# Kernel optimization log

Hardware: AMD Instinct MI355X
Metric: run time of the kernel (lower is better)

## Reference

```python
import jax, jax.numpy as jnp
import numpy as np

B, T, K, U, C, M, H = 64, 600, 10, 64, 54, 20, 512
OUT = 1 + 6 * M        # 121
IN1 = 3 + C            # 57  -> rnn_cell1 input
IN2 = 3 + C + H        # 569 -> rnn_cell2 input
BIAS = 0.0
EPS = 1e-20


def setup_inputs() -> dict:
    key = jax.random.key(0)
    ks = jax.random.split(key, 20)
    p = lambda k, shape: (jax.random.normal(k, shape, dtype=jnp.float32) * 0.05)
    return {
        "x": jax.random.normal(ks[0], (B, T, 3), dtype=jnp.float32),
        "y": jax.random.uniform(ks[1], (B, T, 3), dtype=jnp.float32),
        "c_vec": jax.random.uniform(ks[2], (B, U, C), dtype=jnp.float32),
        "W_ih1": p(ks[3], (4 * H, IN1)), "W_hh1": p(ks[4], (4 * H, H)),
        "b_ih1": p(ks[5], (4 * H,)),     "b_hh1": p(ks[6], (4 * H,)),
        "W_ih2": p(ks[7], (4 * H, IN2)), "W_hh2": p(ks[8], (4 * H, H)),
        "b_ih2": p(ks[9], (4 * H,)),     "b_hh2": p(ks[10], (4 * H,)),
        "W_k": p(ks[11], (3 * K, H)),    "b_k": p(ks[12], (3 * K,)),
        "W_o": p(ks[13], (OUT, H)),      "b_o": p(ks[14], (OUT,)),
    }


def _lstm_cell(xin, h, c, Wih, Whh, bih, bhh):
    g = xin @ Wih.T + h @ Whh.T + bih + bhh          # [B, 4H]
    i, f, gg, o = jnp.split(g, 4, axis=1)            # PyTorch LSTMCell gate order
    c = jax.nn.sigmoid(f) * c + jax.nn.sigmoid(i) * jnp.tanh(gg)
    h = jax.nn.sigmoid(o) * jnp.tanh(c)
    return h, c


def _forward(x, y, c_vec, W_ih1, W_hh1, b_ih1, b_hh1, W_ih2, W_hh2, b_ih2, b_hh2,
             W_k, b_k, W_o, b_o):
    u = jnp.arange(U, dtype=jnp.float32)[None, None, :]   # [1,1,U]
    zB = jnp.zeros((B, H), dtype=x.dtype)

    def step(carry, xt):
        h1, c1, h2, c2, w, kappa = carry
        h1, c1 = _lstm_cell(jnp.concatenate([xt, w], 1), h1, c1, W_ih1, W_hh1, b_ih1, b_hh1)
        kg = h1 @ W_k.T + b_k                               # [B, 3K]
        a_hat, be_hat, ka_hat = jnp.split(kg, 3, axis=1)
        alpha = jnp.exp(a_hat)[:, :, None]                  # [B,K,1]
        beta = jnp.exp(be_hat)[:, :, None]
        kappa = kappa + jnp.exp(ka_hat)[:, :, None]
        phi = jnp.sum(jnp.exp(-beta * (kappa - u) ** 2) * alpha, axis=1)  # [B,U]
        w = jnp.einsum('bu,buc->bc', phi, c_vec)            # [B,C]
        h2, c2 = _lstm_cell(jnp.concatenate([xt, h1, w], 1), h2, c2, W_ih2, W_hh2, b_ih2, b_hh2)
        return (h1, c1, h2, c2, w, kappa), h2

    init = (zB, zB, zB, zB, jnp.zeros((B, C), x.dtype), jnp.zeros((B, K, 1), x.dtype))
    _, h2_seq = jax.lax.scan(step, init, jnp.transpose(x, (1, 0, 2)))   # [T,B,H]
    h2_seq = jnp.transpose(h2_seq, (1, 0, 2)).reshape(-1, H)            # [B*T,H]
    outputs = h2_seq @ W_o.T + b_o                                      # [B*T,OUT]

    y1, y2, s = jnp.moveaxis(y.reshape(-1, 3), 1, 0)                    # each [B*T]
    e = jax.nn.sigmoid(-outputs[:, 0])                                  # 1/(1+exp(o0))
    pi_hat, mu1, mu2, s1_hat, s2_hat, rho_hat = jnp.split(outputs[:, 1:], 6, axis=1)
    pi = jax.nn.softmax(pi_hat, axis=1)
    sigma1 = jnp.exp(s1_hat - BIAS)
    sigma2 = jnp.exp(s2_hat - BIAS)
    rho = jnp.tanh(rho_hat)
    d1 = (y1[:, None] - mu1) / sigma1
    d2 = (y2[:, None] - mu2) / sigma2
    z = d1 ** 2 + d2 ** 2 - 2.0 * rho * d1 * d2
    one_m_r2 = 1.0 - rho ** 2
    gauss = jnp.exp(-z / (2.0 * one_m_r2)) / (2.0 * np.pi * sigma1 * sigma2 * jnp.sqrt(one_m_r2))
    loss_g = jnp.sum(-jnp.log(jnp.sum(pi * gauss, axis=1) + EPS))
    loss_b = jnp.sum(-jnp.log((e + EPS) * s + (1.0 - e + EPS) * (1.0 - s)))
    return (loss_g + loss_b) / (B * T)


def reference(x, y, c_vec, W_ih1, W_hh1, b_ih1, b_hh1, W_ih2, W_hh2, b_ih2, b_hh2,
              W_k, b_k, W_o, b_o):
    return _forward(x, y, c_vec, W_ih1, W_hh1, b_ih1, b_hh1, W_ih2, W_hh2,
                    b_ih2, b_hh2, W_k, b_k, W_o, b_o)
```

## Files before the change

### kernel.cpp

```cpp
#include <hip/hip_runtime.h>
#include <math.h>

typedef _Float16 f16;
typedef _Float16 f16x8 __attribute__((ext_vector_type(8)));
typedef float f32x4 __attribute__((ext_vector_type(4)));
union AFU { unsigned long long q[2]; f16x8 v; };
union HU { f16 h; unsigned short u; };

#define NT 512
#define NBLK 160
#define AROW 1088
#define ABE 69632
#define OUTG_OFF 69632
#define LOSS_OFF 77824
#define BAR_OFF  78080
#define PH_STRIDE 144
#define NPH 1206
#define DYN_LDS 132096

__device__ __forceinline__ unsigned long long ald64(const void* p) {
  return __hip_atomic_load((const unsigned long long*)p, __ATOMIC_RELAXED, __HIP_MEMORY_SCOPE_AGENT);
}
__device__ __forceinline__ unsigned ald32(const void* p) {
  return __hip_atomic_load((const unsigned*)p, __ATOMIC_RELAXED, __HIP_MEMORY_SCOPE_AGENT);
}
__device__ __forceinline__ void ast32(void* p, unsigned v) {
  __hip_atomic_store((unsigned*)p, v, __ATOMIC_RELAXED, __HIP_MEMORY_SCOPE_AGENT);
}
__device__ __forceinline__ float sigm(float v){ return 1.f/(1.f+expf(-v)); }

__device__ __forceinline__ void gbar(unsigned* bar, int p) {
  asm volatile("s_waitcnt vmcnt(0)" ::: "memory");
  __syncthreads();
  if (threadIdx.x == 0) {
    unsigned* base = bar + p * PH_STRIDE;
    unsigned a = __hip_atomic_fetch_add(base + (blockIdx.x & 7) * 16, 1u,
                                        __ATOMIC_RELAXED, __HIP_MEMORY_SCOPE_AGENT);
    if (a == 19u)
      __hip_atomic_fetch_add(base + 128, 1u, __ATOMIC_RELAXED, __HIP_MEMORY_SCOPE_AGENT);
    while (__hip_atomic_load(base + 128, __ATOMIC_RELAXED, __HIP_MEMORY_SCOPE_AGENT) < 8u) {}
  }
  __syncthreads();
}

__device__ __forceinline__ float mix_loss(const float* so, const float* yl, int t, int m) {
  float y1 = yl[t*3+0], y2 = yl[t*3+1], ys = yl[t*3+2];
  float ph = (m < 20) ? so[1+m] : -1e30f;
  float mx = ph;
  #pragma unroll
  for (int d = 16; d >= 1; d >>= 1) mx = fmaxf(mx, __shfl_xor(mx, d));
  float pe = (m < 20) ? expf(ph - mx) : 0.f;
  float ps = pe;
  #pragma unroll
  for (int d = 16; d >= 1; d >>= 1) ps += __shfl_xor(ps, d);
  float contrib = 0.f;
  if (m < 20) {
    float mu1 = so[21+m], mu2 = so[41+m];
    float s1 = expf(so[61+m]), s2 = expf(so[81+m]);
    float rh = tanhf(so[101+m]);
    float d1 = (y1-mu1)/s1, d2 = (y2-mu2)/s2;
    float omr = 1.f - rh*rh;
    float z = d1*d1 + d2*d2 - 2.f*rh*d1*d2;
    float ga = expf(-z/(2.f*omr)) / (6.283185307179586f * s1 * s2 * sqrtf(omr));
    contrib = (pe/ps)*ga;
  }
  float gs = contrib;
  #pragma unroll
  for (int d = 16; d >= 1; d >>= 1) gs += __shfl_xor(gs, d);
  float lg = -logf(gs + 1e-20f);
  float e = 1.f/(1.f + expf(so[0]));
  float lb = -logf((e + 1e-20f)*ys + (1.f - e + 1e-20f)*(1.f - ys));
  return lg + lb;
}

__global__ __launch_bounds__(256) void k_init(float* ws) {
  unsigned* w0 = (unsigned*)ws;
  unsigned* wb = (unsigned*)ws + BAR_OFF;
  int idx = blockIdx.x*256 + threadIdx.x;
  int str = gridDim.x*256;
  for (int e = idx; e < ABE; e += str) w0[e] = 0u;
  for (int e = idx; e < NPH*PH_STRIDE; e += str) wb[e] = 0u;
}

__global__ __launch_bounds__(NT, 1) void kmain(
    const float* __restrict__ x, const float* __restrict__ y, const float* __restrict__ cvec,
    const float* __restrict__ Wih1, const float* __restrict__ Whh1,
    const float* __restrict__ bih1, const float* __restrict__ bhh1,
    const float* __restrict__ Wih2, const float* __restrict__ Whh2,
    const float* __restrict__ bih2, const float* __restrict__ bhh2,
    const float* __restrict__ Wk, const float* __restrict__ bk,
    const float* __restrict__ Wo, const float* __restrict__ bo,
    float* __restrict__ out, float* __restrict__ ws)
{
  extern __shared__ char dsm[];
  const int blk = blockIdx.x, tid = threadIdx.x;
  const int wv = tid >> 6, l = tid & 63;

  f16* AB = (f16*)ws;
  float* outg  = ws + OUTG_OFF;
  float* lossg = ws + LOSS_OFF;
  unsigned* bar = (unsigned*)ws + BAR_OFF;

  float lreg = 0.f;

  if (blk < 64) {
    f16* wf2 = (f16*)dsm;
    for (int f = tid; f < 2*34*64; f += NT) {
      int nt = f / (34*64), rem = f - nt*34*64, j = rem >> 6, lf = rem & 63;
      int nrow = nt*16 + (lf & 15);
      int R = (nrow >> 3)*512 + blk*8 + (nrow & 7);
      int kbase = j*32 + (lf >> 4)*8;
      #pragma unroll
      for (int e = 0; e < 8; ++e) {
        int k = kbase + e;
        float v = 0.f;
        if (k >= 4 && k < 58)        v = Wih2[R*569 + 515 + (k-4)];
        else if (k >= 58 && k < 61)  v = Wih2[R*569 + (k-58)];
        else if (k >= 64 && k < 576) v = Wih2[R*569 + 3 + (k-64)];
        else if (k >= 576)           v = Whh2[R*512 + (k-576)];
        wf2[f*8 + e] = (f16)v;
      }
    }
  } else if (blk < 96) {
    const int g1i = blk - 64;
    f16* wf1  = (f16*)dsm;
    f16* wofr = (f16*)(dsm + 73728);
    for (int f = tid; f < 4*18*64; f += NT) {
      int nt = f / (18*64), rem = f - nt*18*64, j = rem >> 6, lf = rem & 63;
      int nrow = nt*16 + (lf & 15);
      int R = (nrow >> 4)*512 + g1i*16 + (nrow & 15);
      int kbase = j*32 + (lf >> 4)*8;
      #pragma unroll
      for (int e = 0; e < 8; ++e) {
        int k = kbase + e;
        float v = 0.f;
        if (k < 3)                   v = Wih1[R*57 + k];
        else if (k >= 4 && k < 58)   v = Wih1[R*57 + 3 + (k-4)];
        else if (k >= 64 && k < 576) v = Whh1[R*512 + (k-64)];
        wf1[f*8 + e] = (f16)v;
      }
    }
    for (int f = tid; f < 16*64; f += NT) {
      int j = f >> 6, lf = f & 63;
      int nrow = lf & 15, row = g1i*4 + nrow;
      int kbase = j*32 + (lf >> 4)*8;
      #pragma unroll
      for (int e = 0; e < 8; ++e) {
        float v = (nrow < 4 && row < 121) ? Wo[row*512 + kbase + e] : 0.f;
        wofr[f*8 + e] = (f16)v;
      }
    }
  } else {
    const int b = blk - 96;
    f16*   wk  = (f16*)dsm;
    float* cv  = (float*)(dsm + 31200);
    float* xl  = (float*)(dsm + 45024);
    float* yl  = (float*)(dsm + 52224);
    for (int e = tid; e < 30*512; e += NT) { int j = e >> 9, k = e & 511; wk[j*520 + k] = (f16)Wk[e]; }
    for (int e = tid; e < 3456; e += NT) cv[e] = cvec[b*3456 + e];
    for (int e = tid; e < 1800; e += NT) { xl[e] = x[b*1800+e]; yl[e] = y[b*1800+e]; }
    float* kap = (float*)(dsm + 61152);
    if (tid < 10) kap[tid] = 0.f;
    __syncthreads();
    if (tid == 0) {
      HU h0, h1u, h2u;
      h0.h = (f16)xl[0]; h1u.h = (f16)xl[1]; h2u.h = (f16)xl[2];
      ast32((unsigned*)AB + (b*1088 >> 1),       (unsigned)h0.u | ((unsigned)h1u.u << 16));
      ast32((unsigned*)AB + ((b*1088 + 2) >> 1), (unsigned)h2u.u);
    }
  }

  float bias_g[4] = {0,0,0,0}, bias1a[4] = {0,0,0,0}, bias1b[4] = {0,0,0,0};
  float borow = 0.f;
  float c_st = 0.f, c1a = 0.f, c1b = 0.f;
  if (blk < 64) {
    int pr = tid & 7;
    #pragma unroll
    for (int g = 0; g < 4; ++g) {
      int R = g*512 + blk*8 + pr;
      bias_g[g] = bih2[R] + bhh2[R];
    }
  } else if (blk < 96) {
    int g1i = blk - 64, pr = tid & 7;
    #pragma unroll
    for (int g = 0; g < 4; ++g) {
      int Ra = g*512 + g1i*16 + 2*pr, Rb = Ra + 1;
      bias1a[g] = bih1[Ra] + bhh1[Ra];
      bias1b[g] = bih1[Rb] + bhh1[Rb];
    }
    int r = tid >> 6;
    if (r < 4) { int row = g1i*4 + r; borow = (row < 121) ? bo[row] : 0.f; }
  }

  gbar(bar, 0);

  for (int i = 0; i <= 601; ++i) {
    const f16* __restrict__ Acur = AB + (i & 1)*ABE;
    f16* __restrict__ Anxt = AB + ((i & 1)^1)*ABE;
    unsigned* AnxtW = (unsigned*)Anxt;

    if (blk < 64) {
      if (i >= 1 && i <= 600) {
        f16* wf2 = (f16*)dsm;
        float* part2 = (float*)(dsm + 69632);
        const int mt = wv & 3, kh = wv >> 2;
        const int mA = mt*16 + (l & 15);
        const int kb = (l >> 4)*8;
        const f16* Ap = Acur + mA*1088;
        f32x4 acc0 = {0,0,0,0}, acc1 = {0,0,0,0};
        #pragma unroll
        for (int jj = 0; jj < 17; ++jj) {
          int j = kh*17 + jj;
          int k = j*32 + kb;
          AFU af;
          af.q[0] = ald64(Ap + k);
          af.q[1] = ald64(Ap + k + 4);
          f16x8 b0 = *(const f16x8*)&wf2[((0*34 + j)*64 + l)*8];
          f16x8 b1 = *(const f16x8*)&wf2[((1*34 + j)*64 + l)*8];
          acc0 = __builtin_amdgcn_mfma_f32_16x16x32_f16(af.v, b0, acc0, 0, 0, 0);
          acc1 = __builtin_amdgcn_mfma_f32_16x16x32_f16(af.v, b1, acc1, 0, 0, 0);
        }
        #pragma unroll
        for (int r = 0; r < 4; ++r) {
          int m = mt*16 + (l>>4)*4 + r;
          part2[(kh*64 + m)*33 + (l & 15)]      = acc0[r];
          part2[(kh*64 + m)*33 + 16 + (l & 15)] = acc1[r];
        }
        __syncthreads();
        {
          int b_ = tid >> 3, pr = tid & 7;
          const float* p0 = &part2[(0*64 + b_)*33];
          const float* p1 = &part2[(1*64 + b_)*33];
          float gi_ = p0[0*8+pr] + p1[0*8+pr] + bias_g[0];
          float gf_ = p0[1*8+pr] + p1[1*8+pr] + bias_g[1];
          float gg_ = p0[2*8+pr] + p1[2*8+pr] + bias_g[2];
          float go_ = p0[3*8+pr] + p1[3*8+pr] + bias_g[3];
          float ig = sigm(gi_), fg = sigm(gf_), gg2 = tanhf(gg_), og = sigm(go_);
          c_st = fg*c_st + ig*gg2;
          HU hu; hu.h = (f16)(og * tanhf(c_st));
          unsigned myv = hu.u;
          unsigned other = (unsigned)__shfl_xor((int)myv, 1);
          if ((pr & 1) == 0)
            ast32(AnxtW + ((b_*1088 + 576 + blk*8 + pr) >> 1), myv | (other << 16));
        }
      }
    } else if (blk < 96) {
      const int g1i = blk - 64;
      f16* wf1  = (f16*)dsm;
      f16* wofr = (f16*)(dsm + 73728);
      float* part1 = (float*)(dsm + 90112);
      float* partp = (float*)(dsm + 123392);
      bool do_g1 = (i <= 599), do_pr = (i >= 2);
      const int mt = wv & 3, kh = wv >> 2;
      const int mA = mt*16 + (l & 15);
      const int kb = (l >> 4)*8;
      if (do_g1) {
        const f16* Ap = Acur + mA*1088;
        f32x4 acc[4];
        #pragma unroll
        for (int nt = 0; nt < 4; ++nt) acc[nt] = (f32x4){0,0,0,0};
        #pragma unroll
        for (int jj = 0; jj < 9; ++jj) {
          int j = kh*9 + jj;
          int k = j*32 + kb;
          AFU af;
          af.q[0] = ald64(Ap + k);
          af.q[1] = ald64(Ap + k + 4);
          #pragma unroll
          for (int nt = 0; nt < 4; ++nt) {
            f16x8 bf = *(const f16x8*)&wf1[((nt*18 + j)*64 + l)*8];
            acc[nt] = __builtin_amdgcn_mfma_f32_16x16x32_f16(af.v, bf, acc[nt], 0, 0, 0);
          }
        }
        #pragma unroll
        for (int nt = 0; nt < 4; ++nt)
          #pragma unroll
          for (int r = 0; r < 4; ++r) {
            int m = mt*16 + (l>>4)*4 + r;
            part1[(kh*64 + m)*65 + nt*16 + (l & 15)] = acc[nt][r];
          }
      }
      if (do_pr) {
        const f16* Ap = Acur + mA*1088 + 576;
        f32x4 accp = {0,0,0,0};
        #pragma unroll
        for (int jj = 0; jj < 8; ++jj) {
          int j = kh*8 + jj;
          int k = j*32 + kb;
          AFU af;
          af.q[0] = ald64(Ap + k);
          af.q[1] = ald64(Ap + k + 4);
          f16x8 bf = *(const f16x8*)&wofr[(j*64 + l)*8];
          accp = __builtin_amdgcn_mfma_f32_16x16x32_f16(af.v, bf, accp, 0, 0, 0);
        }
        #pragma unroll
        for (int r = 0; r < 4; ++r) {
          int m = mt*16 + (l>>4)*4 + r;
          partp[(kh*64 + m)*17 + (l & 15)] = accp[r];
        }
      }
      if (do_g1 || do_pr) __syncthreads();
      if (do_g1) {
        int b_ = tid >> 3, pr = tid & 7;
        const float* p0 = &part1[(0*64 + b_)*65];
        const float* p1 = &part1[(1*64 + b_)*65];
        float giA = p0[0*16+2*pr] + p1[0*16+2*pr] + bias1a[0];
        float gfA = p0[1*16+2*pr] + p1[1*16+2*pr] + bias1a[1];
        float ggA = p0[2*16+2*pr] + p1[2*16+2*pr] + bias1a[2];
        float goA = p0[3*16+2*pr] + p1[3*16+2*pr] + bias1a[3];
        c1a = sigm(gfA)*c1a + sigm(giA)*tanhf(ggA);
        float hA = sigm(goA) * tanhf(c1a);
        float giB = p0[0*16+2*pr+1] + p1[0*16+2*pr+1] + bias1b[0];
        float gfB = p0[1*16+2*pr+1] + p1[1*16+2*pr+1] + bias1b[1];
        float ggB = p0[2*16+2*pr+1] + p1[2*16+2*pr+1] + bias1b[2];
        float goB = p0[3*16+2*pr+1] + p1[3*16+2*pr+1] + bias1b[3];
        c1b = sigm(gfB)*c1b + sigm(giB)*tanhf(ggB);
        float hB = sigm(goB) * tanhf(c1b);
        HU ua, ub; ua.h = (f16)hA; ub.h = (f16)hB;
        ast32(AnxtW + ((b_*1088 + 64 + g1i*16 + 2*pr) >> 1),
              (unsigned)ua.u | ((unsigned)ub.u << 16));
      }
      if (do_pr && tid < 256) {
        int b_ = tid & 63, r = tid >> 6;
        int row = g1i*4 + r;
        if (row < 121) {
          float v = partp[(0*64 + b_)*17 + r] + partp[(1*64 + b_)*17 + r] + borow;
          unsigned uu; __builtin_memcpy(&uu, &v, 4);
          ast32((unsigned*)outg + b_*128 + row, uu);
        }
      }
    }
    gbar(bar, 1 + 2*i);

    if (blk >= 96) {
      const int b = blk - 96;
      f16*   wk   = (f16*)dsm;
      float* cv   = (float*)(dsm + 31200);
      float* xl   = (float*)(dsm + 45024);
      float* yl   = (float*)(dsm + 52224);
      f16*   h1h  = (f16*)(dsm + 59424);
      float* so   = (float*)(dsm + 60448);
      float* skg  = (float*)(dsm + 60944);
      float* sal  = (float*)(dsm + 61072);
      float* sbe  = (float*)(dsm + 61112);
      float* kap  = (float*)(dsm + 61152);
      float* sphi = (float*)(dsm + 61192);
      float* wtmp = (float*)(dsm + 61448);
      if (i <= 599) {
        if (tid < 64)
          ((unsigned long long*)h1h)[tid] = ald64(Anxt + b*1088 + 64 + tid*4);
        __syncthreads();
        {
          int j = tid >> 4, ksv = tid & 15;
          float a = 0.f;
          if (j < 30) {
            const f16* wr = &wk[j*520 + ksv*32];
            const f16* hr = &h1h[ksv*32];
            #pragma unroll
            for (int c = 0; c < 4; ++c) {
              f16x8 q = *(const f16x8*)(wr + c*8);
              f16x8 h = *(const f16x8*)(hr + c*8);
              #pragma unroll
              for (int e = 0; e < 8; ++e) a += (float)q[e] * (float)h[e];
            }
          }
          a += __shfl_xor(a, 1); a += __shfl_xor(a, 2);
          a += __shfl_xor(a, 4); a += __shfl_xor(a, 8);
          if (j < 30 && ksv == 0) skg[j] = a + bk[j];
        }
        __syncthreads();
        if (tid < 10) {
          sal[tid] = expf(skg[tid]);
          sbe[tid] = expf(skg[10+tid]);
          kap[tid] += expf(skg[20+tid]);
        }
        __syncthreads();
        if (tid < 64) {
          float u = (float)tid, ph = 0.f;
          #pragma unroll
          for (int k2 = 0; k2 < 10; ++k2) {
            float d = kap[k2] - u;
            ph += sal[k2]*expf(-sbe[k2]*d*d);
          }
          sphi[tid] = ph;
        }
        __syncthreads();
        if (tid < 54) {
          float wvv = 0.f;
          #pragma unroll 8
          for (int u = 0; u < 64; ++u) wvv += sphi[u]*cv[u*54 + tid];
          wtmp[tid] = wvv;
        }
        __syncthreads();
        if (tid < 27) {
          HU a, bu; a.h = (f16)wtmp[2*tid]; bu.h = (f16)wtmp[2*tid+1];
          ast32(AnxtW + ((b*1088 + 4 + 2*tid) >> 1), (unsigned)a.u | ((unsigned)bu.u << 16));
        } else if (tid == 27) {
          HU a, bu; a.h = (f16)xl[i*3+0]; bu.h = (f16)xl[i*3+1];
          ast32(AnxtW + ((b*1088 + 58) >> 1), (unsigned)a.u | ((unsigned)bu.u << 16));
        } else if (tid == 28) {
          HU a; a.h = (f16)xl[i*3+2];
          ast32(AnxtW + ((b*1088 + 60) >> 1), (unsigned)a.u);
        } else if (tid == 29 && i <= 598) {
          HU a, bu; a.h = (f16)xl[(i+1)*3+0]; bu.h = (f16)xl[(i+1)*3+1];
          ast32(AnxtW + ((b*1088) >> 1), (unsigned)a.u | ((unsigned)bu.u << 16));
        } else if (tid == 30 && i <= 598) {
          HU a; a.h = (f16)xl[(i+1)*3+2];
          ast32(AnxtW + ((b*1088 + 2) >> 1), (unsigned)a.u);
        }
      }
      if (i >= 2) {
        if (tid < 121) {
          unsigned uu = ald32((unsigned*)outg + b*128 + tid);
          float v; __builtin_memcpy(&v, &uu, 4);
          so[tid] = v;
        }
        __syncthreads();
        if (tid < 32) {
          float v = mix_loss(so, yl, i-2, tid);
          if (tid == 0) lreg += v;
        }
      }
    }
    gbar(bar, 2 + 2*i);
  }

  if (blk >= 96 && tid == 0) {
    unsigned uu; __builtin_memcpy(&uu, &lreg, 4);
    ast32((unsigned*)lossg + (blk - 96), uu);
  }
  gbar(bar, 1205);
  if (blk == 96 && tid < 64) {
    unsigned uu = ald32((unsigned*)lossg + tid);
    float v; __builtin_memcpy(&v, &uu, 4);
    #pragma unroll
    for (int d = 32; d >= 1; d >>= 1) v += __shfl_xor(v, d);
    if (tid == 0) out[0] = v / 38400.f;
  }
}

extern "C" void kernel_launch(void* const* d_in, const int* in_sizes, int n_in,
                              void* d_out, int out_size, void* d_ws, size_t ws_size,
                              hipStream_t stream)
{
  (void)in_sizes; (void)n_in; (void)out_size; (void)ws_size;
  const float* x    = (const float*)d_in[0];
  const float* y    = (const float*)d_in[1];
  const float* cvec = (const float*)d_in[2];
  const float* Wih1 = (const float*)d_in[3];
  const float* Whh1 = (const float*)d_in[4];
  const float* bih1 = (const float*)d_in[5];
  const float* bhh1 = (const float*)d_in[6];
  const float* Wih2 = (const float*)d_in[7];
  const float* Whh2 = (const float*)d_in[8];
  const float* bih2 = (const float*)d_in[9];
  const float* bhh2 = (const float*)d_in[10];
  const float* Wk   = (const float*)d_in[11];
  const float* bk   = (const float*)d_in[12];
  const float* Wo   = (const float*)d_in[13];
  const float* bo   = (const float*)d_in[14];
  float* out = (float*)d_out;
  float* wsf = (float*)d_ws;

  hipFuncSetAttribute((const void*)kmain, hipFuncAttributeMaxDynamicSharedMemorySize, DYN_LDS);

  k_init<<<256, 256, 0, stream>>>(wsf);

  void* args[] = {
    (void*)&x, (void*)&y, (void*)&cvec,
    (void*)&Wih1, (void*)&Whh1, (void*)&bih1, (void*)&bhh1,
    (void*)&Wih2, (void*)&Whh2, (void*)&bih2, (void*)&bhh2,
    (void*)&Wk, (void*)&bk, (void*)&Wo, (void*)&bo,
    (void*)&out, (void*)&wsf
  };
  hipLaunchCooperativeKernel((void*)kmain, dim3(NBLK), dim3(NT), args, DYN_LDS, stream);
}
```

Measured before the change: 10.71 ms.

## Replace atomic counter grid barrier with per-block flag array and batched coherent loads

Swaps the hierarchical fetch-add grid barrier for a per-block monotonically increasing flag that every block polls with vectorized cache-bypassing loads. The relaxed 64-bit atomic loads of activations become 128-bit loads with sc0 sc1 bits, all issued before a single wait so the MFMA loops no longer stall on each load. Stores also use inline-asm coherent stores. The aim is to cut barrier latency and global-load latency on the 1200-step recurrent critical path. The cost is more polling traffic per barrier and reliance on inline-asm cache bits for coherence.

```diff
diff --git a/kernel.cpp b/kernel.cpp
--- a/kernel.cpp
+++ b/kernel.cpp
@@ -4,41 +4,54 @@
 typedef _Float16 f16;
 typedef _Float16 f16x8 __attribute__((ext_vector_type(8)));
 typedef float f32x4 __attribute__((ext_vector_type(4)));
-union AFU { unsigned long long q[2]; f16x8 v; };
 union HU { f16 h; unsigned short u; };
 
 #define NT 512
 #define NBLK 160
-#define AROW 1088
 #define ABE 69632
 #define OUTG_OFF 69632
 #define LOSS_OFF 77824
-#define BAR_OFF  78080
-#define PH_STRIDE 144
-#define NPH 1206
+#define FLAG_OFF 78080
 #define DYN_LDS 132096
 
-__device__ __forceinline__ unsigned long long ald64(const void* p) {
-  return __hip_atomic_load((const unsigned long long*)p, __ATOMIC_RELAXED, __HIP_MEMORY_SCOPE_AGENT);
-}
-__device__ __forceinline__ unsigned ald32(const void* p) {
-  return __hip_atomic_load((const unsigned*)p, __ATOMIC_RELAXED, __HIP_MEMORY_SCOPE_AGENT);
-}
-__device__ __forceinline__ void ast32(void* p, unsigned v) {
-  __hip_atomic_store((unsigned*)p, v, __ATOMIC_RELAXED, __HIP_MEMORY_SCOPE_AGENT);
-}
+__device__ __forceinline__ f16x8 cld16(const void* p) {
+  f16x8 r;
+  asm volatile("global_load_dwordx4 %0, %1, off sc0 sc1" : "=v"(r) : "v"(p) : "memory");
+  return r;
+}
+__device__ __forceinline__ uint4 cld128u(const void* p) {
+  uint4 r;
+  asm volatile("global_load_dwordx4 %0, %1, off sc0 sc1"
+               : "=v"(r) : "v"(p) : "memory");
+  return r;
+}
+__device__ __forceinline__ unsigned cld32u(const void* p) {
+  unsigned r;
+  asm volatile("global_load_dword %0, %1, off sc0 sc1" : "=v"(r) : "v"(p) : "memory");
+  return r;
+}
+__device__ __forceinline__ void cst32(void* p, unsigned v) {
+  asm volatile("global_store_dword %0, %1, off sc0 sc1" :: "v"(p), "v"(v) : "memory");
+}
+#define VMWAIT() do { asm volatile("s_waitcnt vmcnt(0)" ::: "memory"); \
+                      __builtin_amdgcn_sched_barrier(0); } while (0)
+
 __device__ __forceinline__ float sigm(float v){ return 1.f/(1.f+expf(-v)); }
 
-__device__ __forceinline__ void gbar(unsigned* bar, int p) {
+__device__ __forceinline__ void gbar(unsigned* flags, unsigned target) {
   asm volatile("s_waitcnt vmcnt(0)" ::: "memory");
   __syncthreads();
-  if (threadIdx.x == 0) {
-    unsigned* base = bar + p * PH_STRIDE;
-    unsigned a = __hip_atomic_fetch_add(base + (blockIdx.x & 7) * 16, 1u,
-                                        __ATOMIC_RELAXED, __HIP_MEMORY_SCOPE_AGENT);
-    if (a == 19u)
-      __hip_atomic_fetch_add(base + 128, 1u, __ATOMIC_RELAXED, __HIP_MEMORY_SCOPE_AGENT);
-    while (__hip_atomic_load(base + 128, __ATOMIC_RELAXED, __HIP_MEMORY_SCOPE_AGENT) < 8u) {}
+  if (threadIdx.x == 0) cst32(flags + blockIdx.x, target);
+  if (threadIdx.x < 64) {
+    bool ok;
+    do {
+      uint4 vv; vv.x = vv.y = vv.z = vv.w = target;
+      if (threadIdx.x < 40) {
+        vv = cld128u(flags + threadIdx.x * 4);
+        asm volatile("s_waitcnt vmcnt(0)" ::: "memory");
+      }
+      ok = (vv.x >= target) && (vv.y >= target) && (vv.z >= target) && (vv.w >= target);
+    } while (!__all(ok));
   }
   __syncthreads();
 }
@@ -75,11 +88,11 @@
 
 __global__ __launch_bounds__(256) void k_init(float* ws) {
   unsigned* w0 = (unsigned*)ws;
-  unsigned* wb = (unsigned*)ws + BAR_OFF;
+  unsigned* wb = (unsigned*)ws + FLAG_OFF;
   int idx = blockIdx.x*256 + threadIdx.x;
   int str = gridDim.x*256;
   for (int e = idx; e < ABE; e += str) w0[e] = 0u;
-  for (int e = idx; e < NPH*PH_STRIDE; e += str) wb[e] = 0u;
+  if (idx < NBLK) wb[idx] = 0u;
 }
 
 __global__ __launch_bounds__(NT, 1) void kmain(
@@ -99,7 +112,7 @@
   f16* AB = (f16*)ws;
   float* outg  = ws + OUTG_OFF;
   float* lossg = ws + LOSS_OFF;
-  unsigned* bar = (unsigned*)ws + BAR_OFF;
+  unsigned* flags = (unsigned*)ws + FLAG_OFF;
 
   float lreg = 0.f;
 
@@ -165,8 +178,8 @@
     if (tid == 0) {
       HU h0, h1u, h2u;
       h0.h = (f16)xl[0]; h1u.h = (f16)xl[1]; h2u.h = (f16)xl[2];
-      ast32((unsigned*)AB + (b*1088 >> 1),       (unsigned)h0.u | ((unsigned)h1u.u << 16));
-      ast32((unsigned*)AB + ((b*1088 + 2) >> 1), (unsigned)h2u.u);
+      cst32((unsigned*)AB + (b*1088 >> 1),       (unsigned)h0.u | ((unsigned)h1u.u << 16));
+      cst32((unsigned*)AB + ((b*1088 + 2) >> 1), (unsigned)h2u.u);
     }
   }
 
@@ -192,7 +205,7 @@
     if (r < 4) { int row = g1i*4 + r; borow = (row < 121) ? bo[row] : 0.f; }
   }
 
-  gbar(bar, 0);
+  gbar(flags, 1);
 
   for (int i = 0; i <= 601; ++i) {
     const f16* __restrict__ Acur = AB + (i & 1)*ABE;
@@ -208,17 +221,20 @@
         const int kb = (l >> 4)*8;
         const f16* Ap = Acur + mA*1088;
         f32x4 acc0 = {0,0,0,0}, acc1 = {0,0,0,0};
+        f16x8 fr[17];
         #pragma unroll
         for (int jj = 0; jj < 17; ++jj) {
           int j = kh*17 + jj;
-          int k = j*32 + kb;
-          AFU af;
-          af.q[0] = ald64(Ap + k);
-          af.q[1] = ald64(Ap + k + 4);
+          fr[jj] = cld16(Ap + j*32 + kb);
+        }
+        VMWAIT();
+        #pragma unroll
+        for (int jj = 0; jj < 17; ++jj) {
+          int j = kh*17 + jj;
           f16x8 b0 = *(const f16x8*)&wf2[((0*34 + j)*64 + l)*8];
           f16x8 b1 = *(const f16x8*)&wf2[((1*34 + j)*64 + l)*8];
-          acc0 = __builtin_amdgcn_mfma_f32_16x16x32_f16(af.v, b0, acc0, 0, 0, 0);
-          acc1 = __builtin_amdgcn_mfma_f32_16x16x32_f16(af.v, b1, acc1, 0, 0, 0);
+          acc0 = __builtin_amdgcn_mfma_f32_16x16x32_f16(fr[jj], b0, acc0, 0, 0, 0);
+          acc1 = __builtin_amdgcn_mfma_f32_16x16x32_f16(fr[jj], b1, acc1, 0, 0, 0);
         }
         #pragma unroll
         for (int r = 0; r < 4; ++r) {
@@ -241,7 +257,7 @@
           unsigned myv = hu.u;
           unsigned other = (unsigned)__shfl_xor((int)myv, 1);
           if ((pr & 1) == 0)
-            ast32(AnxtW + ((b_*1088 + 576 + blk*8 + pr) >> 1), myv | (other << 16));
+            cst32(AnxtW + ((b_*1088 + 576 + blk*8 + pr) >> 1), myv | (other << 16));
         }
       }
     } else if (blk < 96) {
@@ -254,22 +270,35 @@
       const int mt = wv & 3, kh = wv >> 2;
       const int mA = mt*16 + (l & 15);
       const int kb = (l >> 4)*8;
+      f16x8 fr1[9], frp[8];
       if (do_g1) {
         const f16* Ap = Acur + mA*1088;
-        f32x4 acc[4];
-        #pragma unroll
-        for (int nt = 0; nt < 4; ++nt) acc[nt] = (f32x4){0,0,0,0};
         #pragma unroll
         for (int jj = 0; jj < 9; ++jj) {
           int j = kh*9 + jj;
-          int k = j*32 + kb;
-          AFU af;
-          af.q[0] = ald64(Ap + k);
-          af.q[1] = ald64(Ap + k + 4);
+          fr1[jj] = cld16(Ap + j*32 + kb);
+        }
+      }
+      if (do_pr) {
+        const f16* Ap = Acur + mA*1088 + 576;
+        #pragma unroll
+        for (int jj = 0; jj < 8; ++jj) {
+          int j = kh*8 + jj;
+          frp[jj] = cld16(Ap + j*32 + kb);
+        }
+      }
+      VMWAIT();
+      if (do_g1) {
+        f32x4 acc[4];
+        #pragma unroll
+        for (int nt = 0; nt < 4; ++nt) acc[nt] = (f32x4){0,0,0,0};
+        #pragma unroll
+        for (int jj = 0; jj < 9; ++jj) {
+          int j = kh*9 + jj;
           #pragma unroll
           for (int nt = 0; nt < 4; ++nt) {
             f16x8 bf = *(const f16x8*)&wf1[((nt*18 + j)*64 + l)*8];
-            acc[nt] = __builtin_amdgcn_mfma_f32_16x16x32_f16(af.v, bf, acc[nt], 0, 0, 0);
+            acc[nt] = __builtin_amdgcn_mfma_f32_16x16x32_f16(fr1[jj], bf, acc[nt], 0, 0, 0);
           }
         }
         #pragma unroll
@@ -281,17 +310,12 @@
           }
       }
       if (do_pr) {
-        const f16* Ap = Acur + mA*1088 + 576;
         f32x4 accp = {0,0,0,0};
         #pragma unroll
         for (int jj = 0; jj < 8; ++jj) {
           int j = kh*8 + jj;
-          int k = j*32 + kb;
-          AFU af;
-          af.q[0] = ald64(Ap + k);
-          af.q[1] = ald64(Ap + k + 4);
           f16x8 bf = *(const f16x8*)&wofr[(j*64 + l)*8];
-          accp = __builtin_amdgcn_mfma_f32_16x16x32_f16(af.v, bf, accp, 0, 0, 0);
+          accp = __builtin_amdgcn_mfma_f32_16x16x32_f16(frp[jj], bf, accp, 0, 0, 0);
         }
         #pragma unroll
         for (int r = 0; r < 4; ++r) {
@@ -317,7 +341,7 @@
         c1b = sigm(gfB)*c1b + sigm(giB)*tanhf(ggB);
         float hB = sigm(goB) * tanhf(c1b);
         HU ua, ub; ua.h = (f16)hA; ub.h = (f16)hB;
-        ast32(AnxtW + ((b_*1088 + 64 + g1i*16 + 2*pr) >> 1),
+        cst32(AnxtW + ((b_*1088 + 64 + g1i*16 + 2*pr) >> 1),
               (unsigned)ua.u | ((unsigned)ub.u << 16));
       }
       if (do_pr && tid < 256) {
@@ -326,11 +350,11 @@
         if (row < 121) {
           float v = partp[(0*64 + b_)*17 + r] + partp[(1*64 + b_)*17 + r] + borow;
           unsigned uu; __builtin_memcpy(&uu, &v, 4);
-          ast32((unsigned*)outg + b_*128 + row, uu);
-        }
-      }
-    }
-    gbar(bar, 1 + 2*i);
+          cst32((unsigned*)outg + b_*128 + row, uu);
+        }
+      }
+    }
+    gbar(flags, 2 + 2*i);
 
     if (blk >= 96) {
       const int b = blk - 96;
@@ -347,8 +371,11 @@
       float* sphi = (float*)(dsm + 61192);
       float* wtmp = (float*)(dsm + 61448);
       if (i <= 599) {
-        if (tid < 64)
-          ((unsigned long long*)h1h)[tid] = ald64(Anxt + b*1088 + 64 + tid*4);
+        if (tid < 64) {
+          f16x8 hv = cld16(Anxt + b*1088 + 64 + tid*8);
+          asm volatile("s_waitcnt vmcnt(0)" ::: "memory");
+          *(f16x8*)&h1h[tid*8] = hv;
+        }
         __syncthreads();
         {
           int j = tid >> 4, ksv = tid & 15;
@@ -394,24 +421,25 @@
         __syncthreads();
         if (tid < 27) {
           HU a, bu; a.h = (f16)wtmp[2*tid]; bu.h = (f16)wtmp[2*tid+1];
-          ast32(AnxtW + ((b*1088 + 4 + 2*tid) >> 1), (unsigned)a.u | ((unsigned)bu.u << 16));
+          cst32(AnxtW + ((b*1088 + 4 + 2*tid) >> 1), (unsigned)a.u | ((unsigned)bu.u << 16));
         } else if (tid == 27) {
           HU a, bu; a.h = (f16)xl[i*3+0]; bu.h = (f16)xl[i*3+1];
-          ast32(AnxtW + ((b*1088 + 58) >> 1), (unsigned)a.u | ((unsigned)bu.u << 16));
+          cst32(AnxtW + ((b*1088 + 58) >> 1), (unsigned)a.u | ((unsigned)bu.u << 16));
         } else if (tid == 28) {
           HU a; a.h = (f16)xl[i*3+2];
-          ast32(AnxtW + ((b*1088 + 60) >> 1), (unsigned)a.u);
+          cst32(AnxtW + ((b*1088 + 60) >> 1), (unsigned)a.u);
         } else if (tid == 29 && i <= 598) {
           HU a, bu; a.h = (f16)xl[(i+1)*3+0]; bu.h = (f16)xl[(i+1)*3+1];
-          ast32(AnxtW + ((b*1088) >> 1), (unsigned)a.u | ((unsigned)bu.u << 16));
+          cst32(AnxtW + ((b*1088) >> 1), (unsigned)a.u | ((unsigned)bu.u << 16));
         } else if (tid == 30 && i <= 598) {
           HU a; a.h = (f16)xl[(i+1)*3+2];
-          ast32(AnxtW + ((b*1088 + 2) >> 1), (unsigned)a.u);
+          cst32(AnxtW + ((b*1088 + 2) >> 1), (unsigned)a.u);
         }
       }
       if (i >= 2) {
         if (tid < 121) {
-          unsigned uu = ald32((unsigned*)outg + b*128 + tid);
+          unsigned uu = cld32u((unsigned*)outg + b*128 + tid);
+          asm volatile("s_waitcnt vmcnt(0)" ::: "memory");
           float v; __builtin_memcpy(&v, &uu, 4);
           so[tid] = v;
         }
@@ -422,16 +450,17 @@
         }
       }
     }
-    gbar(bar, 2 + 2*i);
+    gbar(flags, 3 + 2*i);
   }
 
   if (blk >= 96 && tid == 0) {
     unsigned uu; __builtin_memcpy(&uu, &lreg, 4);
-    ast32((unsigned*)lossg + (blk - 96), uu);
-  }
-  gbar(bar, 1205);
+    cst32((unsigned*)lossg + (blk - 96), uu);
+  }
+  gbar(flags, 1206);
   if (blk == 96 && tid < 64) {
-    unsigned uu = ald32((unsigned*)lossg + tid);
+    unsigned uu = cld32u((unsigned*)lossg + tid);
+    asm volatile("s_waitcnt vmcnt(0)" ::: "memory");
     float v; __builtin_memcpy(&v, &uu, 4);
     #pragma unroll
     for (int d = 32; d >= 1; d >>= 1) v += __shfl_xor(v, d);
```

New measurement: 12.01 ms. +12.2%, slower.
